# Optimization experiments

Hardware: AMD Instinct MI355X
Metric: run time of the kernel (lower is better)

## Reference

```python
import jax, jax.numpy as jnp
import numpy as np

N, E, B = 4096, 32768, 1024
NF, EF = 32, 16
ENC, HID, HEADS = 64, 128, 4  # hidden_dim = 2*encoder_dim
MAX_SIZE = 10


def setup_inputs() -> dict:
    key = jax.random.key(0)
    ks = jax.random.split(key, 11)
    return {
        "node_features": jax.random.normal(ks[0], (N, NF), jnp.float32),
        "edge_features": jax.random.normal(ks[1], (E, EF), jnp.float32),
        "edge_index": jax.random.randint(ks[2], (2, E), 0, N, jnp.int32),
        "current_state": jax.random.randint(ks[3], (B,), 0, N, jnp.int32),
        "n_states": jax.random.randint(ks[4], (N,), 1, MAX_SIZE + 1, jnp.int32),
        "W_h": jax.random.normal(ks[5], (NF, HID), jnp.float32) / np.sqrt(NF),
        "W_e": jax.random.normal(ks[6], (EF, HID), jnp.float32) / np.sqrt(EF),
        "W_a": jax.random.normal(ks[7], (5 * HID, HEADS * HID), jnp.float32) / np.sqrt(5 * HID),
        "W_m": jax.random.normal(ks[8], (3 * HID, HEADS * HID), jnp.float32) / np.sqrt(3 * HID),
        "a_kern": jax.random.normal(ks[9], (HID, 1), jnp.float32) / np.sqrt(HID),
        "W_g": jax.random.normal(ks[10], (HID, ENC), jnp.float32) / np.sqrt(HID),
    }


def reference(node_features, edge_features, edge_index, current_state, n_states,
              W_h, W_e, W_a, W_m, a_kern, W_g):
    n_nodes = node_features.shape[0]
    h0 = node_features @ W_h                        # [N, HID]
    e = edge_features @ W_e                         # [E, HID]
    attn_mask = jnp.any(edge_features != 0, axis=-1)  # [E]
    src, tgt = edge_index[0], edge_index[1]
    neg_inf = -jnp.inf
    h = h0
    for i in range(MAX_SIZE):
        node_in = jnp.concatenate([h, h0], axis=-1)  # [N, 2*HID]
        sf = node_in[src]                            # [E, 2*HID]
        tf = node_in[tgt]                            # [E, 2*HID]
        h_a = (jnp.concatenate([sf, e, tf], axis=-1) @ W_a).reshape(-1, HEADS, HID)
        h_m = (jnp.concatenate([e, tf], axis=-1) @ W_m).reshape(-1, HEADS, HID)
        logits = jax.nn.leaky_relu(h_a, 0.2) @ a_kern            # [E, HEADS, 1]
        logits = jnp.where(attn_mask[:, None, None], logits, neg_inf)
        max_per_node = jax.ops.segment_max(logits.reshape(logits.shape[0], -1), src,
                                           num_segments=n_nodes)  # [N, HEADS]
        dead = jnp.isneginf(max_per_node[:, 0])[src]              # [E]
        safe = jnp.where(dead[:, None, None], 0.0, logits)
        # segment softmax over edges grouped by src
        m = jax.ops.segment_max(safe.reshape(-1, HEADS), src, num_segments=n_nodes)
        ex = jnp.exp(safe - m[src][:, :, None])                   # [E, HEADS, 1]
        denom = jax.ops.segment_sum(ex, src, num_segments=n_nodes)
        attn = ex / denom[src]
        msgs = attn * h_m                                         # [E, HEADS, HID]
        agg = jax.ops.segment_sum(msgs, src, num_segments=n_nodes)  # [N, HEADS, HID]
        _h = jnp.tanh(agg.sum(axis=1))                            # [N, HID]
        h = jnp.where((i < n_states)[:, None], _h, h)
    return h[current_state] @ W_g                                 # [B, ENC]
```

## Files before the change

kernel.cpp:

```cpp
#include <hip/hip_runtime.h>
#include <hip/hip_bf16.h>

#define N_NODES 4096
#define N_EDGES 32768
#define BATCH   1024
#define NFEAT   32
#define EFEAT   16
#define ENCD    64
#define HIDD    128
#define HEADS   4
#define HID4    512
#define MAXS    10
#define TVAR    1536

typedef unsigned short ushort_t;
typedef __bf16 bf16x8 __attribute__((ext_vector_type(8)));
typedef float f32x4 __attribute__((ext_vector_type(4)));

static __device__ __forceinline__ float bfbits2f(unsigned int hi16) {
    return __uint_as_float(hi16);
}
static __device__ __forceinline__ void unpack8(uint4 v, float* f) {
    f[0] = bfbits2f(v.x << 16); f[1] = bfbits2f(v.x & 0xffff0000u);
    f[2] = bfbits2f(v.y << 16); f[3] = bfbits2f(v.y & 0xffff0000u);
    f[4] = bfbits2f(v.z << 16); f[5] = bfbits2f(v.z & 0xffff0000u);
    f[6] = bfbits2f(v.w << 16); f[7] = bfbits2f(v.w & 0xffff0000u);
}
static __device__ __forceinline__ void load8bf(const ushort_t* p, float* f) {
    unpack8(*reinterpret_cast<const uint4*>(p), f);
}
static __device__ __forceinline__ unsigned short f2bf(float x) {
    __hip_bfloat16 h = __float2bfloat16(x);
    return *reinterpret_cast<unsigned short*>(&h);
}
static __device__ __forceinline__ unsigned addpack(unsigned s, unsigned a) {
    float s0 = bfbits2f(s << 16), s1 = bfbits2f(s & 0xffff0000u);
    float a0 = bfbits2f(a << 16), a1 = bfbits2f(a & 0xffff0000u);
    unsigned r0 = f2bf(s0 + a0), r1 = f2bf(s1 + a1);
    return r0 | (r1 << 16);
}
static __device__ __forceinline__ uint4 pack8(const float* f) {
    uint4 u;
    u.x = (unsigned)f2bf(f[0]) | ((unsigned)f2bf(f[1]) << 16);
    u.y = (unsigned)f2bf(f[2]) | ((unsigned)f2bf(f[3]) << 16);
    u.z = (unsigned)f2bf(f[4]) | ((unsigned)f2bf(f[5]) << 16);
    u.w = (unsigned)f2bf(f[6]) | ((unsigned)f2bf(f[7]) << 16);
    return u;
}


__global__ void k_zero(int* p) { p[blockIdx.x * blockDim.x + threadIdx.x] = 0; }
__global__ void k_bcount(const int* __restrict__ nst, int* __restrict__ bcnt) {
    int n = blockIdx.x * blockDim.x + threadIdx.x;
    atomicAdd(&bcnt[10 - nst[n]], 1);
}
__global__ void k_bprefix(const int* __restrict__ bcnt, int* __restrict__ bcur,
                          int* __restrict__ cntAct) {
    if (threadIdx.x == 0) {
        int boffs[11]; int run = 0;
        for (int b = 0; b < 10; ++b) { boffs[b] = run; run += bcnt[b]; }
        boffs[10] = run;
        for (int b = 0; b < 10; ++b) bcur[b] = boffs[b];
        for (int i = 0; i < 10; ++i) cntAct[i] = boffs[10 - i];
    }
}
__global__ void k_bscatter(const int* __restrict__ nst, int* __restrict__ bcur,
                           int* __restrict__ perm, int* __restrict__ inv) {
    int n = blockIdx.x * blockDim.x + threadIdx.x;
    int pos = atomicAdd(&bcur[10 - nst[n]], 1);
    perm[pos] = n; inv[n] = pos;
}

__global__ __launch_bounds__(256) void k_comp_eam(const float* __restrict__ We,
                                                  const float* __restrict__ Wa,
                                                  const float* __restrict__ Wm,
                                                  ushort_t* __restrict__ out) {
    __shared__ float w_lds[128][17];
    const int t = threadIdx.x;
    const int p = blockIdx.x;
    const int cl = t & 15, kbase = t >> 4;
    const int c = p * 16 + cl;
#pragma unroll
    for (int i = 0; i < 8; ++i) {
        int kk = kbase + i * 16;
        w_lds[kk][cl] = (c < 512) ? Wa[(256 + kk) * HID4 + c] : Wm[kk * HID4 + (c - 512)];
    }
    __syncthreads();
    const int k = t >> 4;
    float s = 0.f;
    for (int kk = 0; kk < 128; ++kk)
        s = fmaf(We[k * 128 + kk], w_lds[kk][cl], s);
    int l = ((k >> 3) << 4) + cl, j = k & 7;
    out[((size_t)(p * 64 + l)) * 8 + j] = f2bf(s);
    if (t < 32) {
        uint4 z = {0, 0, 0, 0};
        *(uint4*)(out + ((size_t)(p * 64 + 32 + t)) * 8) = z;
    }
}

__global__ __launch_bounds__(256) void k_comp_fix(const float* __restrict__ Wh,
                                                  const float* __restrict__ Wa,
                                                  const float* __restrict__ Wm,
                                                  ushort_t* __restrict__ out) {
    __shared__ float w_lds[128][17];
    const int t = threadIdx.x;
    const int p = blockIdx.x;
    const int cl = t & 15, kbase = t >> 4;
    const int c = p * 16 + cl;
#pragma unroll
    for (int i = 0; i < 8; ++i) {
        int kk = kbase + i * 16;
        w_lds[kk][cl] = (c < 512) ? Wa[(128 + kk) * HID4 + c]
                      : (c < 1024) ? Wa[(512 + kk) * HID4 + (c - 512)]
                                   : Wm[(256 + kk) * HID4 + (c - 1024)];
    }
    __syncthreads();
    const int k1 = t >> 4, k2 = k1 + 16;
    float s1 = 0.f, s2 = 0.f;
    for (int kk = 0; kk < 128; ++kk) {
        float wv = w_lds[kk][cl];
        s1 = fmaf(Wh[k1 * 128 + kk], wv, s1);
        s2 = fmaf(Wh[k2 * 128 + kk], wv, s2);
    }
    int l1 = ((k1 >> 3) << 4) + cl, j1 = k1 & 7;
    int l2 = ((k2 >> 3) << 4) + cl, j2 = k2 & 7;
    out[((size_t)(p * 64 + l1)) * 8 + j1] = f2bf(s1);
    out[((size_t)(p * 64 + l2)) * 8 + j2] = f2bf(s2);
}

__global__ void k_pack_var(const float* __restrict__ Wa, const float* __restrict__ Wm,
                           ushort_t* __restrict__ out) {
    int idx = blockIdx.x * blockDim.x + threadIdx.x;
    int p = idx >> 8, rem = idx & 255;
    int q = rem >> 6, l = rem & 63;
    int c = p * 16 + (l & 15);
    int k0 = q * 32 + ((l >> 4) << 3);
    float v[8];
#pragma unroll
    for (int j = 0; j < 8; ++j) {
        int k = k0 + j;
        v[j] = (c < 512) ? Wa[k * HID4 + c]
             : (c < 1024) ? Wa[(384 + k) * HID4 + (c - 512)]
                          : Wm[(128 + k) * HID4 + (c - 1024)];
    }
    *(uint4*)(out + (size_t)idx * 8) = pack8(v);
}

__global__ void k_prep_ef(const float* __restrict__ ef, const int* __restrict__ eids,
                          ushort_t* __restrict__ out) {
    int idx = blockIdx.x * blockDim.x + threadIdx.x;
    int p = idx >> 6, l = idx & 63;
    int e = eids[p * 16 + (l & 15)];
    int k0 = (l >> 4) << 3;
    float v[8];
#pragma unroll
    for (int j = 0; j < 8; ++j) {
        int k = k0 + j;
        v[j] = (k < 16) ? ef[e * EFEAT + k] : 0.f;
    }
    *(uint4*)(out + (size_t)idx * 8) = pack8(v);
}

__global__ void k_prep_nf(const float* __restrict__ nf, const int* __restrict__ perm,
                          ushort_t* __restrict__ out) {
    int idx = blockIdx.x * blockDim.x + threadIdx.x;
    int p = idx >> 6, l = idx & 63;
    int n = perm[p * 16 + (l & 15)];
    int k0 = (l >> 4) << 3;
    float v[8];
#pragma unroll
    for (int j = 0; j < 8; ++j) v[j] = nf[n * NFEAT + k0 + j];
    *(uint4*)(out + (size_t)idx * 8) = pack8(v);
}

__global__ void k_h0(const float* __restrict__ nf, const float* __restrict__ Wh,
                     const int* __restrict__ inv,
                     float* __restrict__ h, ushort_t* __restrict__ hbf) {
    int idx = blockIdx.x * blockDim.x + threadIdx.x;
    int n = idx >> 7, c = idx & 127;
    float s = 0.f;
#pragma unroll
    for (int k = 0; k < NFEAT; ++k) s += nf[n * NFEAT + k] * Wh[k * HIDD + c];
    int row = inv[n];
    h[(size_t)row * HIDD + c] = s;
    int p = row >> 4, r = row & 15, q = c >> 5, kg = (c >> 3) & 3, j = c & 7;
    hbf[(size_t)(((p * 4 + q) * 64) + kg * 16 + r) * 8 + j] = f2bf(s);
}

__global__ void k_mask(const float* __restrict__ ef, int* __restrict__ mask) {
    int e = blockIdx.x * blockDim.x + threadIdx.x;
    int m = 0;
#pragma unroll
    for (int k = 0; k < EFEAT; ++k) m |= (ef[e * EFEAT + k] != 0.f);
    mask[e] = m;
}

__global__ void k_count(const int* __restrict__ src, const int* __restrict__ inv,
                        int* __restrict__ deg) {
    int e = blockIdx.x * blockDim.x + threadIdx.x;
    atomicAdd(&deg[inv[src[e]]], 1);
}
__global__ __launch_bounds__(1024) void k_scan(const int* __restrict__ deg,
                                               int* __restrict__ offs, int* __restrict__ cursor) {
    __shared__ int sm[1024];
    int t = threadIdx.x;
    int d0 = deg[t * 4], d1 = deg[t * 4 + 1], d2 = deg[t * 4 + 2], d3 = deg[t * 4 + 3];
    int s = d0 + d1 + d2 + d3;
    sm[t] = s; __syncthreads();
    for (int o = 1; o < 1024; o <<= 1) {
        int v = (t >= o) ? sm[t - o] : 0;
        __syncthreads();
        sm[t] += v;
        __syncthreads();
    }
    int run = sm[t] - s;
    offs[t * 4] = run;     cursor[t * 4] = run;     run += d0;
    offs[t * 4 + 1] = run; cursor[t * 4 + 1] = run; run += d1;
    offs[t * 4 + 2] = run; cursor[t * 4 + 2] = run; run += d2;
    offs[t * 4 + 3] = run; cursor[t * 4 + 3] = run;
    if (t == 1023) offs[4096] = run + d3;
}
__global__ void k_fill(const int* __restrict__ src, const int* __restrict__ inv,
                       int* __restrict__ cursor, int* __restrict__ eids) {
    int e = blockIdx.x * blockDim.x + threadIdx.x;
    int pos = atomicAdd(&cursor[inv[src[e]]], 1);
    eids[pos] = e;
}
__global__ void k_tgtp(const int* __restrict__ eids, const int* __restrict__ tgt,
                       const int* __restrict__ inv, const int* __restrict__ mask,
                       int* __restrict__ tgtp, int* __restrict__ maskp) {
    int q = blockIdx.x * blockDim.x + threadIdx.x;
    int e = eids[q];
    tgtp[q] = inv[tgt[e]];
    maskp[q] = mask[e];
}

__global__ __launch_bounds__(256) void k_gemm32(const ushort_t* __restrict__ A_sw,
                                                const ushort_t* __restrict__ B_sw,
                                                ushort_t* __restrict__ C, int NC) {
    __shared__ ushort_t lds[4][64][64];
    const int tid = threadIdx.x;
    const int l = tid & 63;
    const int w = tid >> 6;
    const int mpb = blockIdx.y * 16 + w * 4;
    const int cpb = blockIdx.x * 4;

    bf16x8 a[4], b[4];
#pragma unroll
    for (int mi = 0; mi < 4; ++mi)
        a[mi] = *(const bf16x8*)(A_sw + (size_t)((mpb + mi) * 64 + l) * 8);
#pragma unroll
    for (int ct = 0; ct < 4; ++ct)
        b[ct] = *(const bf16x8*)(B_sw + (size_t)((cpb + ct) * 64 + l) * 8);

    const int rb = (l >> 4) << 2, lc = l & 15;
#pragma unroll
    for (int mi = 0; mi < 4; ++mi)
#pragma unroll
        for (int ct = 0; ct < 4; ++ct) {
            f32x4 c = {0.f, 0.f, 0.f, 0.f};
            c = __builtin_amdgcn_mfma_f32_16x16x32_bf16(a[mi], b[ct], c, 0, 0, 0);
#pragma unroll
            for (int r = 0; r < 4; ++r)
                lds[w][mi * 16 + rb + r][ct * 16 + lc] = f2bf(c[r]);
        }
    __syncthreads();
#pragma unroll
    for (int i = 0; i < 8; ++i) {
        int ch = (i << 6) + l;
        int row = ch >> 3, co = (ch & 7) << 3;
        int grow = blockIdx.y * 256 + w * 64 + row;
        size_t gidx = (size_t)grow * NC + blockIdx.x * 64 + co;
        *(uint4*)(C + gidx) = *(const uint4*)(&lds[w][row][co]);
    }
}

__global__ __launch_bounds__(256) void k_gemm128(const ushort_t* __restrict__ A_sw,
                                                 const ushort_t* __restrict__ B_sw,
                                                 const ushort_t* __restrict__ Cadd,
                                                 ushort_t* __restrict__ C, int NC,
                                                 const int* __restrict__ cntAct, int iter) {
    const int thr = (iter == 0) ? N_NODES : cntAct[iter - 1];
    if ((int)(blockIdx.y * 128) >= thr) return;

    __shared__ ushort_t lds[4][32][64];
    const int tid = threadIdx.x;
    const int l = tid & 63;
    const int w = tid >> 6;
    const int mpb = blockIdx.y * 8 + w * 2;
    const int cpb = blockIdx.x * 4;

    bf16x8 a[2][4], b[4][4];
#pragma unroll
    for (int mi = 0; mi < 2; ++mi)
#pragma unroll
        for (int q = 0; q < 4; ++q)
            a[mi][q] = *(const bf16x8*)(A_sw + (size_t)(((mpb + mi) * 4 + q) * 64 + l) * 8);
#pragma unroll
    for (int ct = 0; ct < 4; ++ct)
#pragma unroll
        for (int q = 0; q < 4; ++q)
            b[ct][q] = *(const bf16x8*)(B_sw + (size_t)(((cpb + ct) * 4 + q) * 64 + l) * 8);

    const int rb = (l >> 4) << 2, lc = l & 15;
#pragma unroll
    for (int mi = 0; mi < 2; ++mi)
#pragma unroll
        for (int ct = 0; ct < 4; ++ct) {
            f32x4 c = {0.f, 0.f, 0.f, 0.f};
#pragma unroll
            for (int q = 0; q < 4; ++q)
                c = __builtin_amdgcn_mfma_f32_16x16x32_bf16(a[mi][q], b[ct][q], c, 0, 0, 0);
#pragma unroll
            for (int r = 0; r < 4; ++r)
                lds[w][mi * 16 + rb + r][ct * 16 + lc] = f2bf(c[r]);
        }
    __syncthreads();
#pragma unroll
    for (int i = 0; i < 4; ++i) {
        int ch = (i << 6) + l;
        int row = ch >> 3, co = (ch & 7) << 3;
        int grow = blockIdx.y * 128 + w * 32 + row;
        size_t gidx = (size_t)grow * NC + blockIdx.x * 64 + co;
        uint4 sv = *(const uint4*)(&lds[w][row][co]);
        uint4 av = *(const uint4*)(Cadd + gidx);
        sv.x = addpack(sv.x, av.x);
        sv.y = addpack(sv.y, av.y);
        sv.z = addpack(sv.z, av.z);
        sv.w = addpack(sv.w, av.w);
        *(uint4*)(C + gidx) = sv;
    }
}

__global__ __launch_bounds__(256) void k_edge(const ushort_t* __restrict__ T,
                                              const ushort_t* __restrict__ eam,
                                              const int* __restrict__ tgtp,
                                              const int* __restrict__ offs,
                                              const int* __restrict__ maskp,
                                              const float* __restrict__ a_kern,
                                              const int* __restrict__ cntAct,
                                              float* __restrict__ h,
                                              ushort_t* __restrict__ hbf, int iter) {
    const int n = (blockIdx.x << 2) + (threadIdx.x >> 6);
    if (n >= cntAct[iter]) return;

    const int lane = threadIdx.x & 63;
    const int c0 = lane << 3;
    const int e0 = offs[n], e1 = offs[n + 1];

    float ak[8];
    {
        const float4* p = reinterpret_cast<const float4*>(a_kern + ((lane & 15) << 3));
        float4 a0 = p[0], a1 = p[1];
        ak[0] = a0.x; ak[1] = a0.y; ak[2] = a0.z; ak[3] = a0.w;
        ak[4] = a1.x; ak[5] = a1.y; ak[6] = a1.z; ak[7] = a1.w;
    }
    float asrc[8];
    load8bf(T + (size_t)n * TVAR + c0, asrc);

    float m = -INFINITY, s = 0.f;
    float acc[8] = {0, 0, 0, 0, 0, 0, 0, 0};

    int mk_n = 0;
    uint4 va_n, vt_n, vm_n, vtm_n;
    if (e0 < e1) {
        int t = tgtp[e0]; mk_n = maskp[e0];
        va_n  = *(const uint4*)(eam + (size_t)e0 * 1024 + c0);
        vt_n  = *(const uint4*)(T + (size_t)t * TVAR + 512 + c0);
        vm_n  = *(const uint4*)(eam + (size_t)e0 * 1024 + 512 + c0);
        vtm_n = *(const uint4*)(T + (size_t)t * TVAR + 1024 + c0);
    }
    for (int q = e0; q < e1; ++q) {
        uint4 va = va_n, vt = vt_n, vm = vm_n, vtm = vtm_n;
        int mk = mk_n;
        int q2 = q + 1;
        if (q2 < e1) {
            int t = tgtp[q2]; mk_n = maskp[q2];
            va_n  = *(const uint4*)(eam + (size_t)q2 * 1024 + c0);
            vt_n  = *(const uint4*)(T + (size_t)t * TVAR + 512 + c0);
            vm_n  = *(const uint4*)(eam + (size_t)q2 * 1024 + 512 + c0);
            vtm_n = *(const uint4*)(T + (size_t)t * TVAR + 1024 + c0);
        }
        float ea[8], tt[8], em[8], tm[8];
        unpack8(va, ea); unpack8(vt, tt); unpack8(vm, em); unpack8(vtm, tm);
        float p = 0.f;
#pragma unroll
        for (int j = 0; j < 8; ++j) {
            float v = asrc[j] + ea[j] + tt[j];
            v = (v > 0.f) ? v : 0.2f * v;
            p = fmaf(v, ak[j], p);
        }
        p += __shfl_xor(p, 1);
        p += __shfl_xor(p, 2);
        p += __shfl_xor(p, 4);
        p += __shfl_xor(p, 8);
        p = mk ? p : -INFINITY;
        float mn = fmaxf(m, p);
        bool live = (mn != -INFINITY);
        float wgt = live ? __expf(p - mn) : 0.f;
        float sc  = live ? __expf(m - mn) : 0.f;
        s = s * sc + wgt;
#pragma unroll
        for (int j = 0; j < 8; ++j) acc[j] = acc[j] * sc + wgt * (em[j] + tm[j]);
        m = mn;
    }
    if (e1 > e0 && m == -INFINITY) {
        s = (float)(e1 - e0);
        for (int q = e0; q < e1; ++q) {
            int t = tgtp[q];
            float em[8], tm[8];
            load8bf(eam + (size_t)q * 1024 + 512 + c0, em);
            load8bf(T + (size_t)t * TVAR + 1024 + c0, tm);
#pragma unroll
            for (int j = 0; j < 8; ++j) acc[j] += em[j] + tm[j];
        }
    }
    float inv_s = (e1 > e0) ? (1.f / s) : 0.f;
    float r[8];
#pragma unroll
    for (int j = 0; j < 8; ++j) {
        float v = acc[j] * inv_s;
        v += __shfl_xor(v, 16);
        v += __shfl_xor(v, 32);
        r[j] = v;
    }
    if (lane < 16) {
        float out[8];
#pragma unroll
        for (int j = 0; j < 8; ++j) out[j] = tanhf(r[j]);
        float4* ph = reinterpret_cast<float4*>(h + (size_t)n * HIDD + c0);
        float4 o0, o1;
        o0.x = out[0]; o0.y = out[1]; o0.z = out[2]; o0.w = out[3];
        o1.x = out[4]; o1.y = out[5]; o1.z = out[6]; o1.w = out[7];
        ph[0] = o0; ph[1] = o1;
        int p = n >> 4, rr = n & 15, q = lane >> 2, kg = lane & 3;
        *(uint4*)(hbf + (size_t)(((p * 4 + q) * 64) + kg * 16 + rr) * 8) = pack8(out);
    }
}

__global__ void k_out(const float* __restrict__ h, const int* __restrict__ cs,
                      const int* __restrict__ inv, const float* __restrict__ Wg,
                      float* __restrict__ out) {
    int idx = blockIdx.x * blockDim.x + threadIdx.x;
    int b = idx >> 6, c = idx & 63;
    int n = inv[cs[b]];
    float s = 0.f;
#pragma unroll
    for (int k = 0; k < HIDD; ++k) s += h[(size_t)n * HIDD + k] * Wg[k * ENCD + c];
    out[idx] = s;
}

extern "C" void kernel_launch(void* const* d_in, const int* in_sizes, int n_in,
                              void* d_out, int out_size, void* d_ws, size_t ws_size,
                              hipStream_t stream) {
    const float* nf  = (const float*)d_in[0];
    const float* ef  = (const float*)d_in[1];
    const int* eidx  = (const int*)d_in[2];
    const int* cs    = (const int*)d_in[3];
    const int* nst   = (const int*)d_in[4];
    const float* Wh  = (const float*)d_in[5];
    const float* We  = (const float*)d_in[6];
    const float* Wa  = (const float*)d_in[7];
    const float* Wm  = (const float*)d_in[8];
    const float* akn = (const float*)d_in[9];
    const float* Wg  = (const float*)d_in[10];
    const int* src = eidx;
    const int* tgt = eidx + N_EDGES;

    char* w = (char*)d_ws;
    size_t off = 0;
    auto alloc = [&](size_t bytes) -> void* {
        void* p = w + off;
        off = (off + bytes + 255) & ~(size_t)255;
        return p;
    };
    float* h         = (float*)alloc((size_t)N_NODES * HIDD * 4);
    ushort_t* hbf    = (ushort_t*)alloc((size_t)N_NODES * HIDD * 2);
    int* mask        = (int*)alloc((size_t)N_EDGES * 4);
    ushort_t* eam    = (ushort_t*)alloc((size_t)N_EDGES * 1024 * 2);
    ushort_t* Tfix   = (ushort_t*)alloc((size_t)N_NODES * TVAR * 2);
    ushort_t* Tcur   = (ushort_t*)alloc((size_t)N_NODES * TVAR * 2);
    ushort_t* Wcomb  = (ushort_t*)alloc((size_t)64 * 64 * 8 * 2);
    ushort_t* WfixC  = (ushort_t*)alloc((size_t)96 * 64 * 8 * 2);
    ushort_t* WvarSw = (ushort_t*)alloc((size_t)96 * 4 * 64 * 8 * 2);
    ushort_t* efp    = (ushort_t*)alloc((size_t)2048 * 64 * 8 * 2);
    ushort_t* nfp    = (ushort_t*)alloc((size_t)256 * 64 * 8 * 2);
    int* iws         = (int*)alloc((size_t)4352 * 4);
    int* deg    = iws;
    int* bcnt   = iws + 4096;
    int* bcur   = iws + 4112;
    int* cntAct = iws + 4128;
    int* offs        = (int*)alloc((size_t)(N_NODES + 1) * 4);
    int* cursor      = (int*)alloc((size_t)N_NODES * 4);
    int* perm        = (int*)alloc((size_t)N_NODES * 4);
    int* inv         = (int*)alloc((size_t)N_NODES * 4);
    int* eids        = (int*)alloc((size_t)N_EDGES * 4);
    int* tgtp        = (int*)alloc((size_t)N_EDGES * 4);
    int* maskp       = (int*)alloc((size_t)N_EDGES * 4);
    (void)ws_size; (void)in_sizes; (void)n_in; (void)out_size;

    k_zero<<<17, 256, 0, stream>>>(iws);
    k_bcount<<<N_NODES / 256, 256, 0, stream>>>(nst, bcnt);
    k_bprefix<<<1, 64, 0, stream>>>(bcnt, bcur, cntAct);
    k_bscatter<<<N_NODES / 256, 256, 0, stream>>>(nst, bcur, perm, inv);
    k_mask<<<N_EDGES / 256, 256, 0, stream>>>(ef, mask);
    k_count<<<N_EDGES / 256, 256, 0, stream>>>(src, inv, deg);
    k_scan<<<1, 1024, 0, stream>>>(deg, offs, cursor);
    k_fill<<<N_EDGES / 256, 256, 0, stream>>>(src, inv, cursor, eids);
    k_tgtp<<<N_EDGES / 256, 256, 0, stream>>>(eids, tgt, inv, mask, tgtp, maskp);

    k_comp_eam<<<64, 256, 0, stream>>>(We, Wa, Wm, Wcomb);
    k_comp_fix<<<96, 256, 0, stream>>>(Wh, Wa, Wm, WfixC);
    k_pack_var<<<96, 256, 0, stream>>>(Wa, Wm, WvarSw);
    k_prep_ef<<<512, 256, 0, stream>>>(ef, eids, efp);
    k_prep_nf<<<64, 256, 0, stream>>>(nf, perm, nfp);
    k_h0<<<(N_NODES * HIDD) / 256, 256, 0, stream>>>(nf, Wh, inv, h, hbf);

    k_gemm32<<<dim3(1024 / 64, N_EDGES / 256), 256, 0, stream>>>(efp, Wcomb, eam, 1024);
    k_gemm32<<<dim3(TVAR / 64, N_NODES / 256), 256, 0, stream>>>(nfp, WfixC, Tfix, TVAR);

    for (int i = 0; i < MAXS; ++i) {
        k_gemm128<<<dim3(TVAR / 64, N_NODES / 128), 256, 0, stream>>>(hbf, WvarSw, Tfix, Tcur,
                                                                      TVAR, cntAct, i);
        k_edge<<<N_NODES / 4, 256, 0, stream>>>(Tcur, eam, tgtp, offs, maskp, akn, cntAct,
                                                h, hbf, i);
    }
    k_out<<<(BATCH * ENCD) / 256, 256, 0, stream>>>(h, cs, inv, Wg, (float*)d_out);
}
```

Measured before the change: 444.6 us.

## Fuse graph preprocessing into one block kernel, fold mask into prep, unroll edge loop

Replaces nine small preprocessing launches (bucket sort, degree count, scan, CSR fill, target permute, mask) with a single 1024-thread block that does everything in shared memory. The edge mask is now computed inside the edge-feature prep kernel using wave shuffles. The per-node edge loop in k_edge is unrolled by two, with a two-edge prefetch and a joint online-softmax update. This cuts launch overhead and global atomics, but the single-block build is serial on one CU and the two-edge unroll raises register pressure.

```diff
diff --git a/kernel.cpp b/kernel.cpp
--- a/kernel.cpp
+++ b/kernel.cpp
@@ -49,26 +49,71 @@
 }
 
 
-__global__ void k_zero(int* p) { p[blockIdx.x * blockDim.x + threadIdx.x] = 0; }
-__global__ void k_bcount(const int* __restrict__ nst, int* __restrict__ bcnt) {
-    int n = blockIdx.x * blockDim.x + threadIdx.x;
-    atomicAdd(&bcnt[10 - nst[n]], 1);
-}
-__global__ void k_bprefix(const int* __restrict__ bcnt, int* __restrict__ bcur,
-                          int* __restrict__ cntAct) {
-    if (threadIdx.x == 0) {
-        int boffs[11]; int run = 0;
-        for (int b = 0; b < 10; ++b) { boffs[b] = run; run += bcnt[b]; }
-        boffs[10] = run;
-        for (int b = 0; b < 10; ++b) bcur[b] = boffs[b];
-        for (int i = 0; i < 10; ++i) cntAct[i] = boffs[10 - i];
-    }
-}
-__global__ void k_bscatter(const int* __restrict__ nst, int* __restrict__ bcur,
-                           int* __restrict__ perm, int* __restrict__ inv) {
-    int n = blockIdx.x * blockDim.x + threadIdx.x;
-    int pos = atomicAdd(&bcur[10 - nst[n]], 1);
-    perm[pos] = n; inv[n] = pos;
+__global__ __launch_bounds__(1024) void k_build(const int* __restrict__ nst,
+                                                const int* __restrict__ src,
+                                                const int* __restrict__ tgt,
+                                                int* __restrict__ perm, int* __restrict__ inv,
+                                                int* __restrict__ offs, int* __restrict__ eids,
+                                                int* __restrict__ tgtp, int* __restrict__ cntAct) {
+    __shared__ int bcnt[16], bcur[16];
+    __shared__ int inv_l[N_NODES];
+    __shared__ int work[N_NODES];
+    __shared__ int ssum[1024];
+    const int t = threadIdx.x;
+    if (t < 16) bcnt[t] = 0;
+    __syncthreads();
+#pragma unroll
+    for (int i = 0; i < 4; ++i) {
+        int n = t + i * 1024;
+        atomicAdd(&bcnt[10 - nst[n]], 1);
+    }
+    __syncthreads();
+    if (t == 0) {
+        int pref[11]; int run = 0;
+        for (int b = 0; b < 10; ++b) { pref[b] = run; run += bcnt[b]; }
+        pref[10] = run;
+        for (int b = 0; b < 10; ++b) bcur[b] = pref[b];
+        for (int i = 0; i < 10; ++i) cntAct[i] = pref[10 - i];
+    }
+    __syncthreads();
+#pragma unroll
+    for (int i = 0; i < 4; ++i) {
+        int n = t + i * 1024;
+        int pos = atomicAdd(&bcur[10 - nst[n]], 1);
+        perm[pos] = n; inv[n] = pos; inv_l[n] = pos;
+    }
+#pragma unroll
+    for (int i = 0; i < 4; ++i) work[t + i * 1024] = 0;
+    __syncthreads();
+#pragma unroll
+    for (int i = 0; i < 32; ++i) {
+        int e = t + i * 1024;
+        atomicAdd(&work[inv_l[src[e]]], 1);
+    }
+    __syncthreads();
+    int d0 = work[t * 4], d1 = work[t * 4 + 1], d2 = work[t * 4 + 2], d3 = work[t * 4 + 3];
+    int s = d0 + d1 + d2 + d3;
+    ssum[t] = s; __syncthreads();
+    for (int o = 1; o < 1024; o <<= 1) {
+        int v = (t >= o) ? ssum[t - o] : 0;
+        __syncthreads();
+        ssum[t] += v;
+        __syncthreads();
+    }
+    int run = ssum[t] - s;
+    offs[t * 4] = run;     work[t * 4] = run;     run += d0;
+    offs[t * 4 + 1] = run; work[t * 4 + 1] = run; run += d1;
+    offs[t * 4 + 2] = run; work[t * 4 + 2] = run; run += d2;
+    offs[t * 4 + 3] = run; work[t * 4 + 3] = run;
+    if (t == 1023) offs[4096] = run + d3;
+    __syncthreads();
+#pragma unroll
+    for (int i = 0; i < 32; ++i) {
+        int e = t + i * 1024;
+        int pos = atomicAdd(&work[inv_l[src[e]]], 1);
+        eids[pos] = e;
+        tgtp[pos] = inv_l[tgt[e]];
+    }
 }
 
 __global__ __launch_bounds__(256) void k_comp_eam(const float* __restrict__ We,
@@ -147,17 +192,23 @@
 }
 
 __global__ void k_prep_ef(const float* __restrict__ ef, const int* __restrict__ eids,
-                          ushort_t* __restrict__ out) {
+                          ushort_t* __restrict__ out, int* __restrict__ maskp) {
     int idx = blockIdx.x * blockDim.x + threadIdx.x;
     int p = idx >> 6, l = idx & 63;
-    int e = eids[p * 16 + (l & 15)];
+    int slot = p * 16 + (l & 15);
+    int e = eids[slot];
     int k0 = (l >> 4) << 3;
     float v[8];
+    int mk = 0;
 #pragma unroll
     for (int j = 0; j < 8; ++j) {
         int k = k0 + j;
         v[j] = (k < 16) ? ef[e * EFEAT + k] : 0.f;
-    }
+        mk |= (v[j] != 0.f);
+    }
+    mk |= __shfl_xor(mk, 16);
+    mk |= __shfl_xor(mk, 32);
+    if ((l >> 4) == 0) maskp[slot] = mk;
     *(uint4*)(out + (size_t)idx * 8) = pack8(v);
 }
 
@@ -185,54 +236,6 @@
     h[(size_t)row * HIDD + c] = s;
     int p = row >> 4, r = row & 15, q = c >> 5, kg = (c >> 3) & 3, j = c & 7;
     hbf[(size_t)(((p * 4 + q) * 64) + kg * 16 + r) * 8 + j] = f2bf(s);
-}
-
-__global__ void k_mask(const float* __restrict__ ef, int* __restrict__ mask) {
-    int e = blockIdx.x * blockDim.x + threadIdx.x;
-    int m = 0;
-#pragma unroll
-    for (int k = 0; k < EFEAT; ++k) m |= (ef[e * EFEAT + k] != 0.f);
-    mask[e] = m;
-}
-
-__global__ void k_count(const int* __restrict__ src, const int* __restrict__ inv,
-                        int* __restrict__ deg) {
-    int e = blockIdx.x * blockDim.x + threadIdx.x;
-    atomicAdd(&deg[inv[src[e]]], 1);
-}
-__global__ __launch_bounds__(1024) void k_scan(const int* __restrict__ deg,
-                                               int* __restrict__ offs, int* __restrict__ cursor) {
-    __shared__ int sm[1024];
-    int t = threadIdx.x;
-    int d0 = deg[t * 4], d1 = deg[t * 4 + 1], d2 = deg[t * 4 + 2], d3 = deg[t * 4 + 3];
-    int s = d0 + d1 + d2 + d3;
-    sm[t] = s; __syncthreads();
-    for (int o = 1; o < 1024; o <<= 1) {
-        int v = (t >= o) ? sm[t - o] : 0;
-        __syncthreads();
-        sm[t] += v;
-        __syncthreads();
-    }
-    int run = sm[t] - s;
-    offs[t * 4] = run;     cursor[t * 4] = run;     run += d0;
-    offs[t * 4 + 1] = run; cursor[t * 4 + 1] = run; run += d1;
-    offs[t * 4 + 2] = run; cursor[t * 4 + 2] = run; run += d2;
-    offs[t * 4 + 3] = run; cursor[t * 4 + 3] = run;
-    if (t == 1023) offs[4096] = run + d3;
-}
-__global__ void k_fill(const int* __restrict__ src, const int* __restrict__ inv,
-                       int* __restrict__ cursor, int* __restrict__ eids) {
-    int e = blockIdx.x * blockDim.x + threadIdx.x;
-    int pos = atomicAdd(&cursor[inv[src[e]]], 1);
-    eids[pos] = e;
-}
-__global__ void k_tgtp(const int* __restrict__ eids, const int* __restrict__ tgt,
-                       const int* __restrict__ inv, const int* __restrict__ mask,
-                       int* __restrict__ tgtp, int* __restrict__ maskp) {
-    int q = blockIdx.x * blockDim.x + threadIdx.x;
-    int e = eids[q];
-    tgtp[q] = inv[tgt[e]];
-    maskp[q] = mask[e];
 }
 
 __global__ __launch_bounds__(256) void k_gemm32(const ushort_t* __restrict__ A_sw,
@@ -332,6 +335,23 @@
     }
 }
 
+#define PREF(qa)                                                                  \
+    do {                                                                          \
+        int _t1 = tgtp[qa]; nmk1 = maskp[qa];                                     \
+        nA1  = *(const uint4*)(eam + (size_t)(qa) * 1024 + c0);                   \
+        nM1  = *(const uint4*)(eam + (size_t)(qa) * 1024 + 512 + c0);             \
+        nT1  = *(const uint4*)(T + (size_t)_t1 * TVAR + 512 + c0);                \
+        nTM1 = *(const uint4*)(T + (size_t)_t1 * TVAR + 1024 + c0);               \
+        int _qb = (qa) + 1;                                                       \
+        if (_qb < e1) {                                                           \
+            int _t2 = tgtp[_qb]; nmk2 = maskp[_qb];                               \
+            nA2  = *(const uint4*)(eam + (size_t)_qb * 1024 + c0);                \
+            nM2  = *(const uint4*)(eam + (size_t)_qb * 1024 + 512 + c0);          \
+            nT2  = *(const uint4*)(T + (size_t)_t2 * TVAR + 512 + c0);            \
+            nTM2 = *(const uint4*)(T + (size_t)_t2 * TVAR + 1024 + c0);           \
+        } else { nmk2 = 0; nA2 = nA1; nM2 = nM1; nT2 = nT1; nTM2 = nTM1; }        \
+    } while (0)
+
 __global__ __launch_bounds__(256) void k_edge(const ushort_t* __restrict__ T,
                                               const ushort_t* __restrict__ eam,
                                               const int* __restrict__ tgtp,
@@ -361,47 +381,45 @@
     float m = -INFINITY, s = 0.f;
     float acc[8] = {0, 0, 0, 0, 0, 0, 0, 0};
 
-    int mk_n = 0;
-    uint4 va_n, vt_n, vm_n, vtm_n;
-    if (e0 < e1) {
-        int t = tgtp[e0]; mk_n = maskp[e0];
-        va_n  = *(const uint4*)(eam + (size_t)e0 * 1024 + c0);
-        vt_n  = *(const uint4*)(T + (size_t)t * TVAR + 512 + c0);
-        vm_n  = *(const uint4*)(eam + (size_t)e0 * 1024 + 512 + c0);
-        vtm_n = *(const uint4*)(T + (size_t)t * TVAR + 1024 + c0);
-    }
-    for (int q = e0; q < e1; ++q) {
-        uint4 va = va_n, vt = vt_n, vm = vm_n, vtm = vtm_n;
-        int mk = mk_n;
-        int q2 = q + 1;
-        if (q2 < e1) {
-            int t = tgtp[q2]; mk_n = maskp[q2];
-            va_n  = *(const uint4*)(eam + (size_t)q2 * 1024 + c0);
-            vt_n  = *(const uint4*)(T + (size_t)t * TVAR + 512 + c0);
-            vm_n  = *(const uint4*)(eam + (size_t)q2 * 1024 + 512 + c0);
-            vtm_n = *(const uint4*)(T + (size_t)t * TVAR + 1024 + c0);
+    uint4 nA1, nM1, nT1, nTM1, nA2, nM2, nT2, nTM2;
+    int nmk1 = 0, nmk2 = 0;
+    if (e0 < e1) PREF(e0);
+
+    for (int q = e0; q < e1; q += 2) {
+        uint4 A1 = nA1, M1 = nM1, T1 = nT1, TM1 = nTM1;
+        uint4 A2 = nA2, M2 = nM2, T2 = nT2, TM2 = nTM2;
+        int mk1 = nmk1, mk2 = nmk2;
+        int qn = q + 2;
+        if (qn < e1) PREF(qn);
+
+        float ea1[8], tt1[8], em1[8], tm1[8], ea2[8], tt2[8], em2[8], tm2[8];
+        unpack8(A1, ea1); unpack8(T1, tt1); unpack8(M1, em1); unpack8(TM1, tm1);
+        unpack8(A2, ea2); unpack8(T2, tt2); unpack8(M2, em2); unpack8(TM2, tm2);
+        float p1 = 0.f, p2 = 0.f;
+#pragma unroll
+        for (int j = 0; j < 8; ++j) {
+            float v1 = asrc[j] + ea1[j] + tt1[j];
+            float v2 = asrc[j] + ea2[j] + tt2[j];
+            v1 = (v1 > 0.f) ? v1 : 0.2f * v1;
+            v2 = (v2 > 0.f) ? v2 : 0.2f * v2;
+            p1 = fmaf(v1, ak[j], p1);
+            p2 = fmaf(v2, ak[j], p2);
         }
-        float ea[8], tt[8], em[8], tm[8];
-        unpack8(va, ea); unpack8(vt, tt); unpack8(vm, em); unpack8(vtm, tm);
-        float p = 0.f;
-#pragma unroll
-        for (int j = 0; j < 8; ++j) {
-            float v = asrc[j] + ea[j] + tt[j];
-            v = (v > 0.f) ? v : 0.2f * v;
-            p = fmaf(v, ak[j], p);
-        }
-        p += __shfl_xor(p, 1);
-        p += __shfl_xor(p, 2);
-        p += __shfl_xor(p, 4);
-        p += __shfl_xor(p, 8);
-        p = mk ? p : -INFINITY;
-        float mn = fmaxf(m, p);
+        p1 += __shfl_xor(p1, 1); p2 += __shfl_xor(p2, 1);
+        p1 += __shfl_xor(p1, 2); p2 += __shfl_xor(p2, 2);
+        p1 += __shfl_xor(p1, 4); p2 += __shfl_xor(p2, 4);
+        p1 += __shfl_xor(p1, 8); p2 += __shfl_xor(p2, 8);
+        p1 = mk1 ? p1 : -INFINITY;
+        p2 = mk2 ? p2 : -INFINITY;
+        float mn = fmaxf(m, fmaxf(p1, p2));
         bool live = (mn != -INFINITY);
-        float wgt = live ? __expf(p - mn) : 0.f;
-        float sc  = live ? __expf(m - mn) : 0.f;
-        s = s * sc + wgt;
-#pragma unroll
-        for (int j = 0; j < 8; ++j) acc[j] = acc[j] * sc + wgt * (em[j] + tm[j]);
+        float w1 = live ? __expf(p1 - mn) : 0.f;
+        float w2 = live ? __expf(p2 - mn) : 0.f;
+        float sc = live ? __expf(m - mn) : 0.f;
+        s = s * sc + w1 + w2;
+#pragma unroll
+        for (int j = 0; j < 8; ++j)
+            acc[j] = acc[j] * sc + w1 * (em1[j] + tm1[j]) + w2 * (em2[j] + tm2[j]);
         m = mn;
     }
     if (e1 > e0 && m == -INFINITY) {
@@ -476,7 +494,6 @@
     };
     float* h         = (float*)alloc((size_t)N_NODES * HIDD * 4);
     ushort_t* hbf    = (ushort_t*)alloc((size_t)N_NODES * HIDD * 2);
-    int* mask        = (int*)alloc((size_t)N_EDGES * 4);
     ushort_t* eam    = (ushort_t*)alloc((size_t)N_EDGES * 1024 * 2);
     ushort_t* Tfix   = (ushort_t*)alloc((size_t)N_NODES * TVAR * 2);
     ushort_t* Tcur   = (ushort_t*)alloc((size_t)N_NODES * TVAR * 2);
@@ -485,34 +502,20 @@
     ushort_t* WvarSw = (ushort_t*)alloc((size_t)96 * 4 * 64 * 8 * 2);
     ushort_t* efp    = (ushort_t*)alloc((size_t)2048 * 64 * 8 * 2);
     ushort_t* nfp    = (ushort_t*)alloc((size_t)256 * 64 * 8 * 2);
-    int* iws         = (int*)alloc((size_t)4352 * 4);
-    int* deg    = iws;
-    int* bcnt   = iws + 4096;
-    int* bcur   = iws + 4112;
-    int* cntAct = iws + 4128;
     int* offs        = (int*)alloc((size_t)(N_NODES + 1) * 4);
-    int* cursor      = (int*)alloc((size_t)N_NODES * 4);
     int* perm        = (int*)alloc((size_t)N_NODES * 4);
     int* inv         = (int*)alloc((size_t)N_NODES * 4);
     int* eids        = (int*)alloc((size_t)N_EDGES * 4);
     int* tgtp        = (int*)alloc((size_t)N_EDGES * 4);
     int* maskp       = (int*)alloc((size_t)N_EDGES * 4);
+    int* cntAct      = (int*)alloc((size_t)16 * 4);
     (void)ws_size; (void)in_sizes; (void)n_in; (void)out_size;
 
-    k_zero<<<17, 256, 0, stream>>>(iws);
-    k_bcount<<<N_NODES / 256, 256, 0, stream>>>(nst, bcnt);
-    k_bprefix<<<1, 64, 0, stream>>>(bcnt, bcur, cntAct);
-    k_bscatter<<<N_NODES / 256, 256, 0, stream>>>(nst, bcur, perm, inv);
-    k_mask<<<N_EDGES / 256, 256, 0, stream>>>(ef, mask);
-    k_count<<<N_EDGES / 256, 256, 0, stream>>>(src, inv, deg);
-    k_scan<<<1, 1024, 0, stream>>>(deg, offs, cursor);
-    k_fill<<<N_EDGES / 256, 256, 0, stream>>>(src, inv, cursor, eids);
-    k_tgtp<<<N_EDGES / 256, 256, 0, stream>>>(eids, tgt, inv, mask, tgtp, maskp);
-
+    k_build<<<1, 1024, 0, stream>>>(nst, src, tgt, perm, inv, offs, eids, tgtp, cntAct);
     k_comp_eam<<<64, 256, 0, stream>>>(We, Wa, Wm, Wcomb);
     k_comp_fix<<<96, 256, 0, stream>>>(Wh, Wa, Wm, WfixC);
     k_pack_var<<<96, 256, 0, stream>>>(Wa, Wm, WvarSw);
-    k_prep_ef<<<512, 256, 0, stream>>>(ef, eids, efp);
+    k_prep_ef<<<512, 256, 0, stream>>>(ef, eids, efp, maskp);
     k_prep_nf<<<64, 256, 0, stream>>>(nf, perm, nfp);
     k_h0<<<(N_NODES * HIDD) / 256, 256, 0, stream>>>(nf, Wh, inv, h, hbf);
 
```

Result: slower. 470.2 us (+5.7%).
